# Kernel tuning notes

Measured on AMD Instinct MI355X. Metric: run time of the kernel, lower is better.

## Reference

```python
import jax, jax.numpy as jnp
import numpy as np

N_NODES = 100000
N_REL = 4
N_EDGES = 400000
IN_F, H_F, OUT_F = 128, 128, 64


def setup_inputs() -> dict:
    key = jax.random.key(0)
    ks = jax.random.split(key, 7)
    x = jax.random.normal(ks[0], (N_NODES, IN_F), dtype=jnp.float32)
    src_idx = jax.random.randint(ks[1], (N_REL, N_EDGES), 0, N_NODES, dtype=jnp.int64)
    dst_idx = jax.random.randint(ks[2], (N_REL, N_EDGES), 0, N_NODES, dtype=jnp.int64)
    # Glorot-ish scale for the per-relation GraphConv weights
    W1 = jax.random.normal(ks[3], (N_REL, IN_F, H_F), dtype=jnp.float32) * (1.0 / np.sqrt(IN_F))
    b1 = jnp.zeros((N_REL, H_F), dtype=jnp.float32)
    W2 = jax.random.normal(ks[4], (N_REL, H_F, OUT_F), dtype=jnp.float32) * (1.0 / np.sqrt(H_F))
    b2 = jnp.zeros((N_REL, OUT_F), dtype=jnp.float32)
    return {"x": x, "src_idx": src_idx, "dst_idx": dst_idx,
            "W1": W1, "b1": b1, "W2": W2, "b2": b2}


def _graph_conv(x, src, dst, W, b):
    """DGL GraphConv with norm='both': out = D_in^{-1/2} A^T D_out^{-1/2} x W + b."""
    n = x.shape[0]
    ones = jnp.ones(src.shape[0], dtype=x.dtype)
    deg_out = jnp.maximum(jax.ops.segment_sum(ones, src, num_segments=n), 1.0)
    deg_in = jnp.maximum(jax.ops.segment_sum(ones, dst, num_segments=n), 1.0)
    xn = x * jax.lax.rsqrt(deg_out)[:, None]              # [N, F] src-side norm
    msg = jnp.take(xn, src, axis=0)                        # [E, F] gather
    agg = jax.ops.segment_sum(msg, dst, num_segments=n)   # [N, F] scatter-add
    agg = agg * jax.lax.rsqrt(deg_in)[:, None]            # dst-side norm
    return agg @ W + b


def _hetero_layer(x, src_idx, dst_idx, Ws, bs):
    # per-relation conv, sum-aggregated across relations (HeteroGraphConv 'sum')
    per_rel = jax.vmap(lambda s, d, W, b: _graph_conv(x, s, d, W, b))(src_idx, dst_idx, Ws, bs)
    return per_rel.sum(axis=0)


def reference(x, src_idx, dst_idx, W1, b1, W2, b2):
    h = jax.nn.relu(_hetero_layer(x, src_idx, dst_idx, W1, b1))
    return _hetero_layer(h, src_idx, dst_idx, W2, b2)
```

## Files before the change

### kernel.cpp

```cpp
#include <hip/hip_runtime.h>
#include <hip/hip_bf16.h>

#define NN 100000
#define NR 4
#define NE 400000
#define INF 128
#define HF 128
#define OUTF 64

#define WIN 16384
#define WIN2 (WIN / 2)
#define NWIN 7
#define SUB 16
#define SLICE (NE / SUB)

#define GB 782
#define P1B 256
#define FGRID (GB + P1B)

#define NBKT 256
#define BKTW 391
#define CAP2 12288

typedef __attribute__((ext_vector_type(8))) short s16x8;
typedef __attribute__((ext_vector_type(4))) float f32x4;

__global__ __launch_bounds__(256) void deg_win_kernel(const int* __restrict__ src,
                                                      const int* __restrict__ dst,
                                                      unsigned int* __restrict__ parts) {
    __shared__ unsigned int hist[WIN2];
    int arr = blockIdx.z;
    int r   = blockIdx.y;
    int win = blockIdx.x / SUB;
    int sub = blockIdx.x % SUB;
    const int4* idx4 = (const int4*)((arr ? dst : src) + (size_t)r * NE + (size_t)sub * SLICE);
    int base = win * WIN;

    uint4 z4 = make_uint4(0, 0, 0, 0);
    for (int i = threadIdx.x; i < WIN2 / 4; i += 256) ((uint4*)hist)[i] = z4;
    __syncthreads();

    auto proc = [&](int4 v) {
        int a;
        a = v.x - base; if ((unsigned)a < WIN) atomicAdd(&hist[a >> 1], 1u << ((a & 1) << 4));
        a = v.y - base; if ((unsigned)a < WIN) atomicAdd(&hist[a >> 1], 1u << ((a & 1) << 4));
        a = v.z - base; if ((unsigned)a < WIN) atomicAdd(&hist[a >> 1], 1u << ((a & 1) << 4));
        a = v.w - base; if ((unsigned)a < WIN) atomicAdd(&hist[a >> 1], 1u << ((a & 1) << 4));
    };

    constexpr int NV = SLICE / 4;
    int i = threadIdx.x;
    for (; i + 256 < NV; i += 512) {
        int4 va = idx4[i];
        int4 vb = idx4[i + 256];
        proc(va);
        proc(vb);
    }
    if (i < NV) proc(idx4[i]);
    __syncthreads();

    unsigned int* outp = parts + ((((size_t)arr * NR + r) * NWIN + win) * SUB + sub) * WIN2;
    for (int j = threadIdx.x; j < WIN2 / 4; j += 256)
        ((uint4*)outp)[j] = ((const uint4*)hist)[j];
}

__global__ void red_norm_kernel(const unsigned int* __restrict__ parts, int* __restrict__ deg_tot,
                                float* __restrict__ rno, float* __restrict__ rni) {
    int n = blockIdx.x * blockDim.x + threadIdx.x;
    if (n >= NN) return;
    if (n == 0) deg_tot[NN] = 0;
    int win = n / WIN, off = n % WIN;
    int word = off >> 1, sh = (off & 1) << 4;
    int tot = 0;
    #pragma unroll
    for (int r = 0; r < NR; r++) {
        const unsigned int* p0 = parts + (((size_t)0 * NR + r) * NWIN + win) * SUB * WIN2 + word;
        const unsigned int* p1 = parts + (((size_t)1 * NR + r) * NWIN + win) * SUB * WIN2 + word;
        int so = 0, si = 0;
        #pragma unroll
        for (int s = 0; s < SUB; s++) {
            so += (p0[(size_t)s * WIN2] >> sh) & 0xFFFFu;
            si += (p1[(size_t)s * WIN2] >> sh) & 0xFFFFu;
        }
        rno[(size_t)r * NN + n] = rsqrtf(fmaxf((float)so, 1.0f));
        rni[(size_t)r * NN + n] = rsqrtf(fmaxf((float)si, 1.0f));
        tot += si;
    }
    deg_tot[n] = tot;
}

__global__ void scan_block_kernel(const int* __restrict__ in, int* __restrict__ out,
                                  int* __restrict__ blockSums, int n) {
    __shared__ int sd[256];
    int t = threadIdx.x;
    int base = blockIdx.x * 1024 + t * 4;
    int v[4];
    #pragma unroll
    for (int j = 0; j < 4; j++) v[j] = (base + j < n) ? ((in[base + j] + 7) & ~7) : 0;
    int ts = v[0] + v[1] + v[2] + v[3];
    sd[t] = ts;
    __syncthreads();
    int acc = ts;
    for (int off = 1; off < 256; off <<= 1) {
        int x = (t >= off) ? sd[t - off] : 0;
        __syncthreads();
        acc += x; sd[t] = acc;
        __syncthreads();
    }
    int run = acc - ts;
    #pragma unroll
    for (int j = 0; j < 4; j++) {
        if (base + j < n) out[base + j] = run;
        run += v[j];
    }
    if (t == 255) blockSums[blockIdx.x] = acc;
}

__global__ void scan_sums_kernel(int* __restrict__ blockSums, int nb) {
    __shared__ int sd[512];
    int t = threadIdx.x;
    int v = (t < nb) ? blockSums[t] : 0;
    sd[t] = v;
    __syncthreads();
    int acc = v;
    for (int off = 1; off < 512; off <<= 1) {
        int x = (t >= off) ? sd[t - off] : 0;
        __syncthreads();
        acc += x; sd[t] = acc;
        __syncthreads();
    }
    if (t < nb) blockSums[t] = acc - v;
}

__global__ void scan_add_kernel(int* __restrict__ row_ptr, const int* __restrict__ blockSums,
                                int* __restrict__ bcur, int n) {
    int i = blockIdx.x * blockDim.x + threadIdx.x;
    if (i < n) {
        int v = row_ptr[i] + blockSums[i >> 10];
        row_ptr[i] = v;
        if (i < NN && (i % BKTW) == 0) bcur[i / BKTW] = v;
    }
}

__global__ void prep_kernel(const float* __restrict__ W1, const float* __restrict__ W2,
                            const float* __restrict__ b1, const float* __restrict__ b2,
                            __hip_bfloat16* __restrict__ Wt1, __hip_bfloat16* __restrict__ Wt2,
                            float* __restrict__ bsum1, float* __restrict__ bsum2) {
    if (blockIdx.x == 384) {
        int t = threadIdx.x;
        if (t < HF) {
            float s = 0.f;
            for (int r = 0; r < NR; r++) s += b1[r * HF + t];
            bsum1[t] = s;
        } else if (t < HF + OUTF) {
            int f = t - HF;
            float s = 0.f;
            for (int r = 0; r < NR; r++) s += b2[r * OUTF + f];
            bsum2[f] = s;
        }
        return;
    }
    int id = blockIdx.x * 256 + threadIdx.x;
    if (id < NR * HF * INF) {
        int r = id >> 14, rem = id & 16383;
        int n_ = rem >> 7, k = rem & 127;
        Wt1[id] = __float2bfloat16(W1[((size_t)r * INF + k) * HF + n_]);
    } else {
        int id2 = id - NR * HF * INF;
        if (id2 < NR * OUTF * HF) {
            int r = id2 >> 13, rem = id2 & 8191;
            int n_ = rem >> 7, k = rem & 127;
            Wt2[id2] = __float2bfloat16(W2[((size_t)r * HF + k) * OUTF + n_]);
        }
    }
}

__device__ __forceinline__ s16x8 pack_bf16x8(float4 a0, float4 a1) {
    union { s16x8 v; __hip_bfloat162 h[4]; } u;
    u.h[0] = __float22bfloat162_rn(make_float2(a0.x, a0.y));
    u.h[1] = __float22bfloat162_rn(make_float2(a0.z, a0.w));
    u.h[2] = __float22bfloat162_rn(make_float2(a1.x, a1.y));
    u.h[3] = __float22bfloat162_rn(make_float2(a1.z, a1.w));
    return u.v;
}

__device__ __forceinline__ void load_lds_16(const void* g, void* l) {
    __builtin_amdgcn_global_load_lds(
        (const __attribute__((address_space(1))) void*)g,
        (__attribute__((address_space(3))) void*)l, 16, 0, 0);
}

template<int F, typename AT>
__device__ __forceinline__ void gemm_body(int mbase, const AT* __restrict__ Xb,
                                          const __hip_bfloat16* __restrict__ Wt,
                                          __hip_bfloat16* __restrict__ Zb, int nrel,
                                          __hip_bfloat16* Bs) {
    constexpr int NT = F / 16;
    constexpr int NG = F * 16;

    int tid  = threadIdx.x;
    int wid  = tid >> 6;
    int lane = tid & 63;
    int quad = lane >> 4;
    int l16  = lane & 15;
    int sw   = l16 & 7;

    int bofs[4];
    #pragma unroll
    for (int kb = 0; kb < 4; kb++)
        bofs[kb] = l16 * 256 + (((kb * 4 + quad) ^ sw) << 4);

    s16x8 afr[2][4];
    #pragma unroll
    for (int mt = 0; mt < 2; mt++) {
        int mrow = mbase + mt * 64 + wid * 16 + l16;
        if (mrow >= NN) mrow = NN - 1;
        #pragma unroll
        for (int kb = 0; kb < 4; kb++) {
            if constexpr (sizeof(AT) == 4) {
                const float* xr = (const float*)Xb + (size_t)mrow * 128 + kb * 32 + quad * 8;
                float4 a0 = *(const float4*)xr;
                float4 a1 = *(const float4*)(xr + 4);
                afr[mt][kb] = pack_bf16x8(a0, a1);
            } else {
                afr[mt][kb] = *(const s16x8*)((const __hip_bfloat16*)Xb + (size_t)mrow * 128 + kb * 32 + quad * 8);
            }
        }
    }

    for (int rel = 0; rel < nrel; rel++) {
        if (rel) __syncthreads();

        {
            const char* W = (const char*)(Wt + (size_t)rel * F * 128);
            #pragma unroll
            for (int it = 0; it < NG / 256; it++) {
                int dg = it * 256 + tid;
                int sg = dg ^ ((dg >> 4) & 7);
                load_lds_16(W + (size_t)sg * 16, (char*)Bs + (size_t)(dg & ~63) * 16);
            }
        }
        __syncthreads();

        __hip_bfloat16* Z = Zb + (size_t)rel * NN * F;

        f32x4 acc[2][NT];
        #pragma unroll
        for (int nt = 0; nt < NT; nt++) {
            acc[0][nt] = (f32x4){0.f, 0.f, 0.f, 0.f};
            acc[1][nt] = (f32x4){0.f, 0.f, 0.f, 0.f};
            #pragma unroll
            for (int kb = 0; kb < 4; kb++) {
                s16x8 bfr = *(const s16x8*)((const char*)Bs + nt * 4096 + bofs[kb]);
                acc[0][nt] = __builtin_amdgcn_mfma_f32_16x16x32_bf16(bfr, afr[0][kb], acc[0][nt], 0, 0, 0);
                acc[1][nt] = __builtin_amdgcn_mfma_f32_16x16x32_bf16(bfr, afr[1][kb], acc[1][nt], 0, 0, 0);
            }
        }

        #pragma unroll
        for (int mt = 0; mt < 2; mt++) {
            int g = mbase + mt * 64 + wid * 16 + l16;
            if (g < NN) {
                #pragma unroll
                for (int nt = 0; nt < NT; nt++) {
                    union { uint2 u; __hip_bfloat162 h[2]; } o;
                    o.h[0] = __float22bfloat162_rn(make_float2(acc[mt][nt][0], acc[mt][nt][1]));
                    o.h[1] = __float22bfloat162_rn(make_float2(acc[mt][nt][2], acc[mt][nt][3]));
                    *(uint2*)(Z + (size_t)g * F + nt * 16 + quad * 4) = o.u;
                }
            }
        }
    }
}

__global__ __launch_bounds__(256, 3) void fusedA_kernel(
        const float* __restrict__ x, const __hip_bfloat16* __restrict__ Wt1,
        __hip_bfloat16* __restrict__ Zb,
        const int* __restrict__ src, const int* __restrict__ dst,
        const float* __restrict__ rno, const float* __restrict__ rni,
        int* __restrict__ bcur, int2* __restrict__ temp) {
    __shared__ __attribute__((aligned(16))) char sm[NBKT * 16 * 8 + NBKT * 4];
    int b = blockIdx.x;
    bool isp = ((b & 3) == 3) && ((b >> 2) < P1B);
    if (!isp) {
        int cnt = (b + 1) >> 2; if (cnt > P1B) cnt = P1B;
        gemm_body<HF, float>((b - cnt) * 128, x, Wt1, Zb, NR, (__hip_bfloat16*)sm);
        return;
    }
    int2 (*lbuf)[16] = (int2(*)[16])sm;
    int* lcur = (int*)(sm + NBKT * 16 * 8);
    int blk = b >> 2;
    int r   = blk >> 6;
    int i0  = (blk & 63) * 6250;
    int tid = threadIdx.x;
    lcur[tid] = 0;
    __syncthreads();
    for (int e0 = 0; e0 < 6250; e0 += 256) {
        int e = e0 + tid;
        if (e < 6250) {
            int s = src[(size_t)r * NE + i0 + e];
            int d = dst[(size_t)r * NE + i0 + e];
            unsigned k = (unsigned)d / BKTW;
            int dlo = d - (int)k * BKTW;
            float c = rno[(size_t)r * NN + s] * rni[(size_t)r * NN + d];
            int2 rec = make_int2(((r * NN + s) << 9) | dlo, __float_as_int(c));
            int pos = atomicAdd(&lcur[k], 1);
            if (pos < 16) lbuf[k][pos] = rec;
            else {
                int g = atomicAdd(&bcur[k], 1);
                temp[g] = rec;
            }
        }
        __syncthreads();
        int fill = lcur[tid]; if (fill > 16) fill = 16;
        int nout = fill & ~7;
        if (nout) {
            int g = atomicAdd(&bcur[tid], nout);
            int2* dq = temp + g;
            for (int j = 0; j < nout; j++) dq[j] = lbuf[tid][j];
            int rem = fill - nout;
            for (int j = 0; j < rem; j++) lbuf[tid][j] = lbuf[tid][nout + j];
            lcur[tid] = rem;
        } else lcur[tid] = fill;
        __syncthreads();
    }
    int fill = lcur[tid]; if (fill > 16) fill = 16;
    if (fill) {
        int g = atomicAdd(&bcur[tid], fill);
        for (int j = 0; j < fill; j++) temp[g + j] = lbuf[tid][j];
    }
}

__global__ __launch_bounds__(256) void pass2_kernel(const int* __restrict__ bcur,
                                                    const int2* __restrict__ temp,
                                                    const int* __restrict__ row_ptr,
                                                    int2* __restrict__ edges) {
    __shared__ __attribute__((aligned(16))) int2 stg[CAP2];
    __shared__ int cur[BKTW + 1];
    int k   = blockIdx.x;
    int D0  = k * BKTW;
    int ND  = NN - D0; if (ND > BKTW) ND = BKTW;
    int base = row_ptr[D0];
    int span = row_ptr[D0 + ND] - base;
    int cnt  = bcur[k] - base;
    int tid  = threadIdx.x;

    if (span <= CAP2) {
        int4 z = make_int4(0, 0, 0, 0);
        for (int j = tid; j < (span >> 1); j += 256) ((int4*)stg)[j] = z;
        for (int i = tid; i < ND; i += 256) cur[i] = row_ptr[D0 + i] - base;
        __syncthreads();
        for (int j = tid; j < cnt; j += 256) {
            int2 rec = temp[base + j];
            int i = rec.x & 511;
            int p = atomicAdd(&cur[i], 1);
            stg[p] = make_int2((rec.x >> 9) << 8, rec.y);
        }
        __syncthreads();
        int4* dq = (int4*)(edges + base);
        const int4* sq = (const int4*)stg;
        for (int j = tid; j < (span >> 1); j += 256) dq[j] = sq[j];
    } else {
        int4 z = make_int4(0, 0, 0, 0);
        int4* dq = (int4*)(edges + base);
        for (int j = tid; j < (span >> 1); j += 256) dq[j] = z;
        for (int i = tid; i < ND; i += 256) cur[i] = row_ptr[D0 + i];
        __syncthreads();
        for (int j = tid; j < cnt; j += 256) {
            int2 rec = temp[base + j];
            int i = rec.x & 511;
            int p = atomicAdd(&cur[i], 1);
            edges[p] = make_int2((rec.x >> 9) << 8, rec.y);
        }
    }
}

template<int F, typename AT>
__global__ __launch_bounds__(256, 3) void gemm_all(const AT* __restrict__ Xb,
                                                   const __hip_bfloat16* __restrict__ Wt,
                                                   __hip_bfloat16* __restrict__ Zb, int nrel) {
    __shared__ __attribute__((aligned(16))) __hip_bfloat16 Bs[F * 128];
    gemm_body<F, AT>(blockIdx.x * 128, Xb, Wt, Zb, nrel, Bs);
}

template<int F, bool RELU, bool OUT_F32>
__global__ __launch_bounds__(256) void gather_merged(const int* __restrict__ row_ptr,
                              const int2* __restrict__ edges,
                              const __hip_bfloat16* __restrict__ Zb,
                              float* __restrict__ outf, __hip_bfloat16* __restrict__ outb,
                              const float* __restrict__ bsum) {
    int wid  = threadIdx.x >> 6;
    int lane = threadIdx.x & 63;
    int n = blockIdx.x * 4 + wid;
    int beg = row_ptr[n];
    int end = row_ptr[n + 1];

    if constexpr (F == 128) {
        const char* Zl = (const char*)Zb + lane * 4;
        float2 a = *(const float2*)(bsum + lane * 2);
        for (int p = beg; p < end; p += 8) {
            int2 e[8];
            #pragma unroll
            for (int j = 0; j < 8; j++) e[j] = edges[p + j];
            float2 zz[8];
            #pragma unroll
            for (int j = 0; j < 8; j++)
                zz[j] = __bfloat1622float2(*(const __hip_bfloat162*)(Zl + e[j].x));
            #pragma unroll
            for (int j = 0; j < 8; j++) {
                float c = __int_as_float(e[j].y);
                a.x = fmaf(c, zz[j].x, a.x);
                a.y = fmaf(c, zz[j].y, a.y);
            }
        }
        if constexpr (RELU) { a.x = fmaxf(a.x, 0.f); a.y = fmaxf(a.y, 0.f); }
        *(__hip_bfloat162*)(outb + (size_t)n * 128 + lane * 2) = __float22bfloat162_rn(a);
    } else {
        const char* Zl = (const char*)Zb + lane * 2;
        float a = bsum[lane];
        for (int p = beg; p < end; p += 8) {
            int2 e[8];
            #pragma unroll
            for (int j = 0; j < 8; j++) e[j] = edges[p + j];
            float zz[8];
            #pragma unroll
            for (int j = 0; j < 8; j++)
                zz[j] = __bfloat162float(*(const __hip_bfloat16*)(Zl + (e[j].x >> 1)));
            #pragma unroll
            for (int j = 0; j < 8; j++) a = fmaf(__int_as_float(e[j].y), zz[j], a);
        }
        if constexpr (RELU) a = fmaxf(a, 0.f);
        if constexpr (OUT_F32) outf[(size_t)n * 64 + lane] = a;
        else outb[(size_t)n * 64 + lane] = __float2bfloat16(a);
    }
}

extern "C" void kernel_launch(void* const* d_in, const int* in_sizes, int n_in,
                              void* d_out, int out_size, void* d_ws, size_t ws_size,
                              hipStream_t stream) {
    const float* x   = (const float*)d_in[0];
    const int*   src = (const int*)  d_in[1];
    const int*   dst = (const int*)  d_in[2];
    const float* W1  = (const float*)d_in[3];
    const float* b1  = (const float*)d_in[4];
    const float* W2  = (const float*)d_in[5];
    const float* b2  = (const float*)d_in[6];
    float* out = (float*)d_out;

    constexpr int RN = NR * NN;
    constexpr int NSC = NN + 1;
    constexpr int NB = (NSC + 1023) / 1024;

    char* p = (char*)d_ws;
    int*   deg_tot   = (int*)p;   p += ((size_t)NN + 16) * 4;
    float* rno       = (float*)p; p += (size_t)RN * 4;
    float* rni       = (float*)p; p += (size_t)RN * 4;
    int*   row_ptr   = (int*)p;   p += ((size_t)NN + 16) * 4;
    int*   cursor    = (int*)p;   p += (size_t)NN * 4;
    int*   blockSums = (int*)p;   p += 1024 * 4;
    int2*  edges     = (int2*)p;  p += ((size_t)NR * NE + 8 * NN) * 8;
    float* bsum1 = (float*)p; p += HF * 4;
    float* bsum2 = (float*)p; p += OUTF * 4;
    __hip_bfloat16* hb  = (__hip_bfloat16*)p; p += (size_t)NN * HF * 2;
    __hip_bfloat16* Wt1 = (__hip_bfloat16*)p; p += (size_t)NR * HF * INF * 2;
    __hip_bfloat16* Wt2 = (__hip_bfloat16*)p; p += (size_t)NR * OUTF * HF * 2;
    __hip_bfloat16* Zb = (__hip_bfloat16*)p;
    unsigned int* parts = (unsigned int*)Zb;
    int* bcur = blockSums + 512;
    int2* temp = (int2*)hb;

    prep_kernel<<<385, 256, 0, stream>>>(W1, W2, b1, b2, Wt1, Wt2, bsum1, bsum2);
    deg_win_kernel<<<dim3(NWIN * SUB, NR, 2), 256, 0, stream>>>(src, dst, parts);
    red_norm_kernel<<<(NN + 255) / 256, 256, 0, stream>>>(parts, deg_tot, rno, rni);
    scan_block_kernel<<<NB, 256, 0, stream>>>(deg_tot, row_ptr, blockSums, NSC);
    scan_sums_kernel<<<1, 512, 0, stream>>>(blockSums, NB);
    scan_add_kernel<<<(NSC + 255) / 256, 256, 0, stream>>>(row_ptr, blockSums, bcur, NSC);

    fusedA_kernel<<<FGRID, 256, 0, stream>>>(x, Wt1, Zb, src, dst, rno, rni, bcur, temp);

    pass2_kernel<<<NBKT, 256, 0, stream>>>(bcur, temp, row_ptr, edges);

    constexpr int GG = NN / 4;

    gather_merged<HF, true, false><<<GG, 256, 0, stream>>>(
        row_ptr, edges, Zb, nullptr, hb, bsum1);

    gemm_all<OUTF, __hip_bfloat16><<<GB, 256, 0, stream>>>(hb, Wt2, Zb, 4);
    gather_merged<OUTF, false, true><<<GG, 256, 0, stream>>>(
        row_ptr, edges, Zb, out, nullptr, bsum2);
}
```

Baseline: 418.9 us.

## Shrink bucketing records and move edge norm computation into pass2

The fused GEMM+bucketing kernel now writes 4-byte records (source index and dest offset) instead of 8-byte records with a precomputed norm coefficient. The rno*rni product is computed later in pass2 from the packed index. The bucketing blocks are also reorganized: 784 small blocks each handle 2048 edges with vectorized int4 loads, interleaved 1:1 with GEMM blocks, and there is a single flush instead of a looped staging scheme. This cuts temp traffic and random gathers in the first pass, at the cost of more global atomics and extra rno/rni gathers in pass2.

```diff
diff --git a/kernel.cpp b/kernel.cpp
--- a/kernel.cpp
+++ b/kernel.cpp
@@ -15,12 +15,15 @@
 #define SLICE (NE / SUB)
 
 #define GB 782
-#define P1B 256
-#define FGRID (GB + P1B)
 
 #define NBKT 256
 #define BKTW 391
+#define CAPB 16
 #define CAP2 12288
+#define EPB 2048
+#define SPR 196
+#define S1B (NR * SPR)
+#define FGRID (GB + S1B)
 
 typedef __attribute__((ext_vector_type(8))) short s16x8;
 typedef __attribute__((ext_vector_type(4))) float f32x4;
@@ -273,67 +276,59 @@
     }
 }
 
-__global__ __launch_bounds__(256, 3) void fusedA_kernel(
+__global__ __launch_bounds__(256, 3) void fusedC_kernel(
         const float* __restrict__ x, const __hip_bfloat16* __restrict__ Wt1,
         __hip_bfloat16* __restrict__ Zb,
         const int* __restrict__ src, const int* __restrict__ dst,
-        const float* __restrict__ rno, const float* __restrict__ rni,
-        int* __restrict__ bcur, int2* __restrict__ temp) {
-    __shared__ __attribute__((aligned(16))) char sm[NBKT * 16 * 8 + NBKT * 4];
+        int* __restrict__ bcur, unsigned int* __restrict__ temp) {
+    __shared__ __attribute__((aligned(16))) char sm[HF * 128 * 2];
     int b = blockIdx.x;
-    bool isp = ((b & 3) == 3) && ((b >> 2) < P1B);
-    if (!isp) {
-        int cnt = (b + 1) >> 2; if (cnt > P1B) cnt = P1B;
-        gemm_body<HF, float>((b - cnt) * 128, x, Wt1, Zb, NR, (__hip_bfloat16*)sm);
+    if ((b & 1) == 0 && (b >> 1) < GB) {
+        gemm_body<HF, float>((b >> 1) * 128, x, Wt1, Zb, NR, (__hip_bfloat16*)sm);
         return;
     }
-    int2 (*lbuf)[16] = (int2(*)[16])sm;
-    int* lcur = (int*)(sm + NBKT * 16 * 8);
-    int blk = b >> 2;
-    int r   = blk >> 6;
-    int i0  = (blk & 63) * 6250;
+    int sb = (b & 1) ? (b >> 1) : (S1B - 1);
+    unsigned int (*lbuf)[CAPB] = (unsigned int(*)[CAPB])sm;
+    int* cur = (int*)(sm + NBKT * CAPB * 4);
+
+    int r = sb / SPR;
+    int q = sb % SPR;
+    int base_e = q * EPB;
+    int n = NE - base_e; if (n > EPB) n = EPB;
     int tid = threadIdx.x;
-    lcur[tid] = 0;
-    __syncthreads();
-    for (int e0 = 0; e0 < 6250; e0 += 256) {
-        int e = e0 + tid;
-        if (e < 6250) {
-            int s = src[(size_t)r * NE + i0 + e];
-            int d = dst[(size_t)r * NE + i0 + e];
+    cur[tid] = 0;
+    __syncthreads();
+
+    if (tid * 8 < n) {
+        const int4* sp4 = (const int4*)(src + (size_t)r * NE + base_e);
+        const int4* dp4 = (const int4*)(dst + (size_t)r * NE + base_e);
+        int4 s0 = sp4[tid * 2], s1 = sp4[tid * 2 + 1];
+        int4 d0 = dp4[tid * 2], d1 = dp4[tid * 2 + 1];
+        auto one = [&](int s, int d) {
             unsigned k = (unsigned)d / BKTW;
             int dlo = d - (int)k * BKTW;
-            float c = rno[(size_t)r * NN + s] * rni[(size_t)r * NN + d];
-            int2 rec = make_int2(((r * NN + s) << 9) | dlo, __float_as_int(c));
-            int pos = atomicAdd(&lcur[k], 1);
-            if (pos < 16) lbuf[k][pos] = rec;
-            else {
-                int g = atomicAdd(&bcur[k], 1);
-                temp[g] = rec;
-            }
-        }
-        __syncthreads();
-        int fill = lcur[tid]; if (fill > 16) fill = 16;
-        int nout = fill & ~7;
-        if (nout) {
-            int g = atomicAdd(&bcur[tid], nout);
-            int2* dq = temp + g;
-            for (int j = 0; j < nout; j++) dq[j] = lbuf[tid][j];
-            int rem = fill - nout;
-            for (int j = 0; j < rem; j++) lbuf[tid][j] = lbuf[tid][nout + j];
-            lcur[tid] = rem;
-        } else lcur[tid] = fill;
-        __syncthreads();
-    }
-    int fill = lcur[tid]; if (fill > 16) fill = 16;
-    if (fill) {
-        int g = atomicAdd(&bcur[tid], fill);
-        for (int j = 0; j < fill; j++) temp[g + j] = lbuf[tid][j];
+            unsigned rec = ((unsigned)(r * NN + s) << 9) | (unsigned)dlo;
+            int pos = atomicAdd(&cur[k], 1);
+            if (pos < CAPB) lbuf[k][pos] = rec;
+            else temp[atomicAdd(&bcur[k], 1)] = rec;
+        };
+        one(s0.x, d0.x); one(s0.y, d0.y); one(s0.z, d0.z); one(s0.w, d0.w);
+        one(s1.x, d1.x); one(s1.y, d1.y); one(s1.z, d1.z); one(s1.w, d1.w);
+    }
+    __syncthreads();
+
+    int c = cur[tid]; if (c > CAPB) c = CAPB;
+    if (c) {
+        int g = atomicAdd(&bcur[tid], c);
+        for (int j = 0; j < c; j++) temp[g + j] = lbuf[tid][j];
     }
 }
 
 __global__ __launch_bounds__(256) void pass2_kernel(const int* __restrict__ bcur,
-                                                    const int2* __restrict__ temp,
+                                                    const unsigned int* __restrict__ temp,
                                                     const int* __restrict__ row_ptr,
+                                                    const float* __restrict__ rno,
+                                                    const float* __restrict__ rni,
                                                     int2* __restrict__ edges) {
     __shared__ __attribute__((aligned(16))) int2 stg[CAP2];
     __shared__ int cur[BKTW + 1];
@@ -351,10 +346,12 @@
         for (int i = tid; i < ND; i += 256) cur[i] = row_ptr[D0 + i] - base;
         __syncthreads();
         for (int j = tid; j < cnt; j += 256) {
-            int2 rec = temp[base + j];
-            int i = rec.x & 511;
-            int p = atomicAdd(&cur[i], 1);
-            stg[p] = make_int2((rec.x >> 9) << 8, rec.y);
+            unsigned rec = temp[base + j];
+            int dlo = rec & 511;
+            unsigned idx = rec >> 9;
+            int p = atomicAdd(&cur[dlo], 1);
+            float c = rno[idx] * rni[(size_t)(idx / NN) * NN + D0 + dlo];
+            stg[p] = make_int2((int)(idx << 8), __float_as_int(c));
         }
         __syncthreads();
         int4* dq = (int4*)(edges + base);
@@ -367,10 +364,12 @@
         for (int i = tid; i < ND; i += 256) cur[i] = row_ptr[D0 + i];
         __syncthreads();
         for (int j = tid; j < cnt; j += 256) {
-            int2 rec = temp[base + j];
-            int i = rec.x & 511;
-            int p = atomicAdd(&cur[i], 1);
-            edges[p] = make_int2((rec.x >> 9) << 8, rec.y);
+            unsigned rec = temp[base + j];
+            int dlo = rec & 511;
+            unsigned idx = rec >> 9;
+            int p = atomicAdd(&cur[dlo], 1);
+            float c = rno[idx] * rni[(size_t)(idx / NN) * NN + D0 + dlo];
+            edges[p] = make_int2((int)(idx << 8), __float_as_int(c));
         }
     }
 }
@@ -467,7 +466,7 @@
     __hip_bfloat16* Zb = (__hip_bfloat16*)p;
     unsigned int* parts = (unsigned int*)Zb;
     int* bcur = blockSums + 512;
-    int2* temp = (int2*)hb;
+    unsigned int* temp = (unsigned int*)hb;
 
     prep_kernel<<<385, 256, 0, stream>>>(W1, W2, b1, b2, Wt1, Wt2, bsum1, bsum2);
     deg_win_kernel<<<dim3(NWIN * SUB, NR, 2), 256, 0, stream>>>(src, dst, parts);
@@ -476,9 +475,9 @@
     scan_sums_kernel<<<1, 512, 0, stream>>>(blockSums, NB);
     scan_add_kernel<<<(NSC + 255) / 256, 256, 0, stream>>>(row_ptr, blockSums, bcur, NSC);
 
-    fusedA_kernel<<<FGRID, 256, 0, stream>>>(x, Wt1, Zb, src, dst, rno, rni, bcur, temp);
-
-    pass2_kernel<<<NBKT, 256, 0, stream>>>(bcur, temp, row_ptr, edges);
+    fusedC_kernel<<<FGRID, 256, 0, stream>>>(x, Wt1, Zb, src, dst, bcur, temp);
+
+    pass2_kernel<<<NBKT, 256, 0, stream>>>(bcur, temp, row_ptr, rno, rni, edges);
 
     constexpr int GG = NN / 4;
 
```

Result: faster. 370.5 us (-11.5%).
